# Kernel tuning notes

Measured on AMD Instinct MI355X. Metric: run time of the kernel, lower is better.

## Reference

```python
import jax, jax.numpy as jnp
import numpy as np

N_NODES = 10000
N_EDGES = 320000


def _segment_softmax(scores, seg, num_segments):
    # scores: [E, H], segment-wise stable softmax keyed by seg (edge_index[0])
    m = jax.ops.segment_max(scores, seg, num_segments=num_segments)
    e = jnp.exp(scores - m[seg])
    z = jax.ops.segment_sum(e, seg, num_segments=num_segments)
    return e / z[seg]


def _gat_layer(x, W, a, row, col, n_nodes, heads, out_dim):
    # x: [N, F_in], W: [F_in, heads*out_dim], a: [heads, 2*out_dim]
    h = (x @ W).reshape(n_nodes, heads, out_dim)          # [N, H, F]
    a_l, a_r = a[:, :out_dim], a[:, out_dim:]             # [H, F] each
    # attention score per edge/head without materializing [E, H, 2F]
    s = (h[row] * a_l).sum(-1) + (h[col] * a_r).sum(-1)   # [E, H]
    alpha = _segment_softmax(s, row, n_nodes)             # [E, H]
    msg = alpha[..., None] * h[row]                       # [E, H, F]
    return jax.ops.segment_sum(msg, col, num_segments=n_nodes)  # [N, H, F]


def setup_inputs() -> dict:
    key = jax.random.key(0)
    ks = jax.random.split(key, 6)
    F, H, C = 128, 4, 22
    x = jax.random.normal(ks[0], (N_NODES, F), dtype=jnp.float32)
    edge_index = jax.random.randint(ks[1], (2, N_EDGES), 0, N_NODES, dtype=jnp.int64)
    W1 = jax.random.normal(ks[2], (F, F * H), dtype=jnp.float32) * 0.05
    a1 = jax.random.normal(ks[3], (H, 2 * F), dtype=jnp.float32) * 0.05
    W2 = jax.random.normal(ks[4], (F, C), dtype=jnp.float32) * 0.05
    a2 = jax.random.normal(ks[5], (1, 2 * C), dtype=jnp.float32) * 0.05
    return {"x": x, "edge_index": edge_index, "W1": W1, "a1": a1, "W2": W2, "a2": a2}


def reference(x, edge_index, W1, a1, W2, a2):
    row, col = edge_index[0], edge_index[1]
    h1 = _gat_layer(x, W1, a1, row, col, N_NODES, heads=4, out_dim=128)  # [N, 4, 128]
    h1 = jax.nn.elu(h1).mean(axis=1)                                      # combine heads -> [N, 128]
    h2 = _gat_layer(h1, W2, a2, row, col, N_NODES, heads=1, out_dim=22)   # [N, 1, 22]
    return h2[:, 0, :]                                                    # [N, 22]
```

## Files before the change

kernel.cpp:

```cpp
#include <hip/hip_runtime.h>

#define NN 10000
#define NE 320000
#define EPP 5000
#define NPART 64

typedef short short8 __attribute__((ext_vector_type(8)));
typedef float f32x4 __attribute__((ext_vector_type(4)));

__device__ __forceinline__ unsigned short f2bf(float f) {
    unsigned u = __float_as_uint(f);
    return (unsigned short)((u + 0x7FFFu + ((u >> 16) & 1u)) >> 16);
}
__device__ __forceinline__ float bflo(unsigned v) { return __uint_as_float(v << 16); }
__device__ __forceinline__ float bfhi(unsigned v) { return __uint_as_float(v & 0xffff0000u); }
__device__ __forceinline__ float bf1(unsigned short v) { return __uint_as_float(((unsigned)v) << 16); }

__device__ __forceinline__ int eread(const void* p, int is64, int i) {
    if (is64) return (int)((const long long*)p)[i];
    return ((const int*)p)[i];
}

__device__ __forceinline__ int detect64(const void* ei) {
    const unsigned* idx = (const unsigned*)ei;
    int all0 = 1;
    for (int j = 1; j < 257; j += 2)
        if (idx[j] != 0u) { all0 = 0; break; }
    return all0;
}

__global__ __launch_bounds__(256) void k_pre(const float* __restrict__ x,
                                             unsigned short* __restrict__ xb,
                                             const void* __restrict__ ei,
                                             unsigned short* __restrict__ degp_c,
                                             unsigned short* __restrict__ degp_r,
                                             unsigned* __restrict__ packed_c,
                                             unsigned* __restrict__ packed_r,
                                             const float* __restrict__ W1, const float* __restrict__ a1,
                                             unsigned short* __restrict__ W1t,
                                             float* __restrict__ wrf) {
    __shared__ int sh[NN];
    const int b = blockIdx.x, t = threadIdx.x;
    if (b < 2500) {
        const int g = b * 256 + t;
        const float2 v = *(const float2*)&x[(size_t)g * 2];
        ushort2 o; o.x = f2bf(v.x); o.y = f2bf(v.y);
        *(ushort2*)&xb[(size_t)g * 2] = o;
    } else if (b < 2500 + 2 * NPART) {
        const int is64 = detect64(ei);
        const int isC = (b < 2500 + NPART);
        const int p = isC ? (b - 2500) : (b - 2500 - NPART);
        const int ebase = p * EPP;
        for (int q = t; q < NN; q += 256) sh[q] = 0;
        __syncthreads();
        if (isC) {
            for (int q = t; q < EPP; q += 256) {
                const int e = ebase + q;
                const int c = eread(ei, is64, NE + e);
                const unsigned rk = (unsigned)atomicAdd(&sh[c], 1);
                packed_c[e] = ((unsigned)c << 13) | rk;
            }
            __syncthreads();
            for (int q = t; q < NN; q += 256) degp_c[p * NN + q] = (unsigned short)sh[q];
        } else {
            for (int q = t; q < EPP; q += 256) {
                const int e = ebase + q;
                const int r = eread(ei, is64, e);
                const unsigned rk = (unsigned)atomicAdd(&sh[r], 1);
                packed_r[e] = ((unsigned)r << 13) | rk;
            }
            __syncthreads();
            for (int q = t; q < NN; q += 256) degp_r[p * NN + q] = (unsigned short)sh[q];
        }
    } else if (b < 2500 + 2 * NPART + 256) {
        const int g = (b - 2500 - 2 * NPART) * 256 + t;
        const int h = g >> 14, j = (g >> 7) & 127, k = g & 127;
        W1t[g] = f2bf(W1[(size_t)k * 512 + h * 128 + j]);
    } else {
        const int g = (b - 2500 - 2 * NPART - 256) * 256 + t;
        const int h = g >> 7, k = g & 127;
        const float* wrow = W1 + (size_t)k * 512 + h * 128;
        const float* av = a1 + h * 256 + 128;
        float s = 0.f;
        for (int d = 0; d < 128; d++) s += wrow[d] * av[d];
        wrf[h * 128 + k] = s;
    }
}

__global__ __launch_bounds__(256) void k_psum(const unsigned short* __restrict__ degp_c,
                                              const unsigned short* __restrict__ degp_r,
                                              unsigned short* __restrict__ pfx_c,
                                              unsigned short* __restrict__ pfx_r,
                                              int* __restrict__ deg_c, int* __restrict__ deg_r) {
    const int g = blockIdx.x * 256 + threadIdx.x;
    if (g >= 2 * NN) return;
    const int arr = g / NN, node = g % NN;
    const unsigned short* degp = arr ? degp_r : degp_c;
    unsigned short* pfx = arr ? pfx_r : pfx_c;
    int* tot = arr ? deg_r : deg_c;
    int sum = 0;
#pragma unroll
    for (int p = 0; p < NPART; p++) {
        pfx[p * NN + node] = (unsigned short)sum;
        sum += (int)degp[p * NN + node];
    }
    tot[node] = sum;
}

__device__ void scan_one_1k(const int* __restrict__ deg, int* __restrict__ start, int* ssum) {
    const int t = threadIdx.x;
    int loc[10];
    const int base = t * 10;
    int sum = 0;
#pragma unroll
    for (int j = 0; j < 10; j++) {
        int i = base + j;
        int v = (i < NN) ? deg[i] : 0;
        loc[j] = sum;
        sum += v;
    }
    const int lane = t & 63, w = t >> 6;
    int xi = sum;
#pragma unroll
    for (int off = 1; off < 64; off <<= 1) {
        int y = __shfl_up(xi, off);
        if (lane >= off) xi += y;
    }
    __syncthreads();
    if (lane == 63) ssum[w] = xi;
    __syncthreads();
    int woff = 0;
#pragma unroll
    for (int k = 0; k < 16; k++)
        if (k < w) woff += ssum[k];
    const int excl = woff + xi - sum;
#pragma unroll
    for (int j = 0; j < 10; j++) {
        int i = base + j;
        if (i < NN) start[i] = excl + loc[j];
    }
}

__global__ __launch_bounds__(1024) void k_scan2(const int* __restrict__ deg_c, const int* __restrict__ deg_r,
                                                int* __restrict__ start_c, int* __restrict__ start_r) {
    __shared__ int ssum[16];
    scan_one_1k(deg_c, start_c, ssum);
    __syncthreads();
    scan_one_1k(deg_r, start_r, ssum);
}

__global__ __launch_bounds__(256) void k_build(const unsigned* __restrict__ packed_c,
                                               const unsigned* __restrict__ packed_r,
                                               const unsigned short* __restrict__ pfx_c,
                                               const unsigned short* __restrict__ pfx_r,
                                               const int* __restrict__ start_c, const int* __restrict__ start_r,
                                               int* __restrict__ csrA, int* __restrict__ csrB,
                                               const float* __restrict__ x, const float* __restrict__ wrf,
                                               float* __restrict__ ehr1) {
    __shared__ float ls[512];
    const int b = blockIdx.x, t = threadIdx.x;
    if (b < 1250) {
        const int e = b * 256 + t;
        const int part = e / EPP;
        const unsigned pc = packed_c[e], pr = packed_r[e];
        const int c = (int)(pc >> 13), rkc = (int)(pc & 8191u);
        const int r = (int)(pr >> 13), rkr = (int)(pr & 8191u);
        csrA[start_c[c] + (int)pfx_c[part * NN + c] + rkc] = r;
        csrB[start_r[r] + (int)pfx_r[part * NN + r] + rkr] = c;
    } else {
        const int lane = t & 63, w = t >> 6;
        ls[t] = wrf[t];
        ls[t + 256] = wrf[t + 256];
        __syncthreads();
        const int i = (b - 1250) * 4 + w;
        const float x0 = x[(size_t)i * 128 + lane];
        const float x1 = x[(size_t)i * 128 + 64 + lane];
        float v[4];
#pragma unroll
        for (int h = 0; h < 4; h++)
            v[h] = x0 * ls[h * 128 + lane] + x1 * ls[h * 128 + 64 + lane];
#pragma unroll
        for (int off = 1; off < 64; off <<= 1) {
#pragma unroll
            for (int j = 0; j < 4; j++) v[j] += __shfl_xor(v[j], off);
        }
        if (lane == 0)
            *(float4*)&ehr1[i * 4] = make_float4(__expf(v[0]), __expf(v[1]), __expf(v[2]), __expf(v[3]));
    }
}

__global__ __launch_bounds__(256) void k_z1(const int* __restrict__ start_r, const int* __restrict__ deg_r,
                                            const int* __restrict__ csrB,
                                            const float* __restrict__ ehr1, float* __restrict__ rz1) {
    const int t = threadIdx.x, lane = t & 63, w = t >> 6;
    const int half = lane >> 5, l32 = lane & 31;
    const int i = blockIdx.x * 8 + w * 2 + half;
    const int s0 = start_r[i], d = deg_r[i];
    float zx = 0.f, zy = 0.f, zz = 0.f, zw = 0.f;
    for (int p = s0 + l32; p < s0 + d; p += 32) {
        const int c = csrB[p];
        const float4 v = *(const float4*)&ehr1[c * 4];
        zx += v.x; zy += v.y; zz += v.z; zw += v.w;
    }
#pragma unroll
    for (int off = 1; off < 32; off <<= 1) {
        zx += __shfl_xor(zx, off); zy += __shfl_xor(zy, off);
        zz += __shfl_xor(zz, off); zw += __shfl_xor(zw, off);
    }
    if (l32 == 0)
        *(float4*)&rz1[i * 4] = make_float4(1.f / zx, 1.f / zy, 1.f / zz, 1.f / zw);
}

__global__ __launch_bounds__(256) void k_aggF(const unsigned short* __restrict__ xb,
                                              const float* __restrict__ ehr1, const float* __restrict__ rz1,
                                              const int* __restrict__ start_c, const int* __restrict__ deg_c,
                                              const int* __restrict__ csrA,
                                              const unsigned short* __restrict__ W1t,
                                              const float* __restrict__ W2, const float* __restrict__ a2,
                                              float* __restrict__ h2, float* __restrict__ ehr2) {
    __shared__ unsigned short lx[16 * 512];
    __shared__ float h1f[16 * 128];
    const int t = threadIdx.x, lane = t & 63, w = t >> 6;
    const int n0 = blockIdx.x * 16;

    {
        const int li = lane & 15, g = lane >> 4;
        const int row = w * 4 + g;
        const int i = n0 + row;
        const float4 er4 = *(const float4*)&ehr1[i * 4];
        const int s0 = start_c[i], dg = deg_c[i];
        int m = dg;
        m = max(m, __shfl_xor(m, 16));
        m = max(m, __shfl_xor(m, 32));
        float acc[4][8];
#pragma unroll
        for (int h = 0; h < 4; h++)
#pragma unroll
            for (int d = 0; d < 8; d++) acc[h][d] = 0.f;
        const int niter = (m + 3) >> 2;
        for (int it = 0; it < niter; ++it) {
            const int base = it * 4;
            int rr[4]; uint4 vv[4]; float4 zz[4];
#pragma unroll
            for (int q = 0; q < 4; q++) {
                int p = s0 + base + q;
                if (p >= NE) p = NE - 1;
                rr[q] = csrA[p];
            }
#pragma unroll
            for (int q = 0; q < 4; q++)
                vv[q] = *(const uint4*)&xb[(size_t)rr[q] * 128 + li * 8];
#pragma unroll
            for (int q = 0; q < 4; q++) {
                const float4 z = *(const float4*)&rz1[rr[q] * 4];
                const bool val = (base + q) < dg;
                zz[q] = val ? z : make_float4(0.f, 0.f, 0.f, 0.f);
            }
#pragma unroll
            for (int q = 0; q < 4; q++) {
                float f[8];
                f[0] = bflo(vv[q].x); f[1] = bfhi(vv[q].x);
                f[2] = bflo(vv[q].y); f[3] = bfhi(vv[q].y);
                f[4] = bflo(vv[q].z); f[5] = bfhi(vv[q].z);
                f[6] = bflo(vv[q].w); f[7] = bfhi(vv[q].w);
                const float wz0 = zz[q].x, wz1 = zz[q].y, wz2 = zz[q].z, wz3 = zz[q].w;
#pragma unroll
                for (int d = 0; d < 8; d++) {
                    acc[0][d] += wz0 * f[d];
                    acc[1][d] += wz1 * f[d];
                    acc[2][d] += wz2 * f[d];
                    acc[3][d] += wz3 * f[d];
                }
            }
        }
        const float ef[4] = {er4.x, er4.y, er4.z, er4.w};
#pragma unroll
        for (int h = 0; h < 4; h++) {
            unsigned o[4];
#pragma unroll
            for (int d2 = 0; d2 < 4; d2++) {
                const unsigned lo = f2bf(acc[h][d2 * 2] * ef[h]);
                const unsigned hi = f2bf(acc[h][d2 * 2 + 1] * ef[h]);
                o[d2] = lo | (hi << 16);
            }
            const int f = h * 16 + li;
            const int sc = (f ^ (row & 7)) << 3;
            *(uint4*)&lx[row * 512 + sc] = make_uint4(o[0], o[1], o[2], o[3]);
        }
    }
    __syncthreads();

    {
        const int r16 = lane & 15, grp = lane >> 4;
#pragma unroll
        for (int jj = 0; jj < 2; jj++) {
            const int j = w * 2 + jj;
            f32x4 hm = (f32x4)0.f;
#pragma unroll
            for (int h = 0; h < 4; h++) {
                f32x4 acc = (f32x4)0.f;
#pragma unroll
                for (int kk = 0; kk < 128; kk += 32) {
                    const int f = h * 16 + (kk >> 3) + grp;
                    const int sc = (f ^ (r16 & 7)) << 3;
                    short8 a = *(const short8*)&lx[r16 * 512 + sc];
                    short8 bfr = *(const short8*)&W1t[(size_t)h * 16384 + (j * 16 + r16) * 128 + kk + grp * 8];
                    acc = __builtin_amdgcn_mfma_f32_16x16x32_bf16(a, bfr, acc, 0, 0, 0);
                }
#pragma unroll
                for (int r = 0; r < 4; r++) {
                    const float v = acc[r];
                    hm[r] += (v > 0.f) ? v : (__expf(v) - 1.f);
                }
            }
#pragma unroll
            for (int r = 0; r < 4; r++)
                h1f[(grp * 4 + r) * 128 + j * 16 + r16] = 0.25f * hm[r];
        }
    }
    __syncthreads();

    {
        const int seg = lane >> 5, c = lane & 31;
#pragma unroll
        for (int q = 0; q < 4; q++) {
            const int nl = w * 4 + q;
            const int i = n0 + nl;
            float part = 0.f;
            if (c < 22) {
                const float* hrow = &h1f[nl * 128 + seg * 64];
                const float* wp = &W2[seg * 64 * 22 + c];
                for (int k = 0; k < 64; k++)
                    part += hrow[k] * wp[k * 22];
            }
            part += __shfl_xor(part, 32);
            if (lane < 22) h2[(size_t)i * 22 + lane] = part;
            float pr = (lane < 22) ? part * a2[22 + lane] : 0.f;
#pragma unroll
            for (int off = 1; off < 64; off <<= 1)
                pr += __shfl_xor(pr, off);
            if (lane == 0) ehr2[i] = __expf(pr);
        }
    }
}

__global__ __launch_bounds__(256) void k_z2s(const int* __restrict__ start_r, const int* __restrict__ deg_r,
                                             const int* __restrict__ csrB,
                                             const float* __restrict__ ehr2, const float* __restrict__ h2,
                                             unsigned short* __restrict__ h2s) {
    const int t = threadIdx.x, lane = t & 63, w = t >> 6;
    const int half = lane >> 5, l32 = lane & 31;
    const int i = blockIdx.x * 8 + w * 2 + half;
    const int s0 = start_r[i], d = deg_r[i];
    float z = 0.f;
    for (int p = s0 + l32; p < s0 + d; p += 32)
        z += ehr2[csrB[p]];
#pragma unroll
    for (int off = 1; off < 32; off <<= 1)
        z += __shfl_xor(z, off);
    const float rz = 1.f / z;
    if (l32 < 22)
        h2s[(size_t)i * 32 + l32] = f2bf(h2[(size_t)i * 22 + l32] * rz);
}

__global__ __launch_bounds__(256) void k_agg2(const unsigned short* __restrict__ h2s,
                                              const float* __restrict__ ehr2,
                                              const int* __restrict__ start_c, const int* __restrict__ deg_c,
                                              const int* __restrict__ csrA,
                                              float* __restrict__ out) {
    const int t = threadIdx.x, lane = t & 63, w = t >> 6;
    const int half = lane >> 5, c32 = lane & 31;
    const int i = blockIdx.x * 8 + w * 2 + half;
    const int s0 = start_c[i], dg = deg_c[i];
    const float e2 = ehr2[i];
    const int c = (c32 < 22) ? c32 : 0;
    float acc = 0.f;
    int p = s0;
    const int e8 = s0 + (dg & ~7);
    for (; p < e8; p += 8) {
        int rr[8];
#pragma unroll
        for (int q = 0; q < 8; q++) rr[q] = csrA[p + q];
        float vv[8];
#pragma unroll
        for (int q = 0; q < 8; q++) vv[q] = bf1(h2s[(size_t)rr[q] * 32 + c]);
#pragma unroll
        for (int q = 0; q < 8; q++) acc += vv[q];
    }
    for (; p < s0 + dg; ++p) {
        const int r = csrA[p];
        acc += bf1(h2s[(size_t)r * 32 + c]);
    }
    if (c32 < 22) out[(size_t)i * 22 + c32] = acc * e2;
}

extern "C" void kernel_launch(void* const* d_in, const int* in_sizes, int n_in,
                              void* d_out, int out_size, void* d_ws, size_t ws_size,
                              hipStream_t stream) {
    const float* x  = (const float*)d_in[0];
    const void*  ei = d_in[1];
    const float* W1 = (const float*)d_in[2];
    const float* a1 = (const float*)d_in[3];
    const float* W2 = (const float*)d_in[4];
    const float* a2 = (const float*)d_in[5];
    float* out = (float*)d_out;

    float* ws = (float*)d_ws;
    float* h2   = ws;
    float* ehr1 = ws + 220000;
    float* rz1  = ws + 260000;
    float* ehr2 = ws + 300000;
    unsigned short* h2s = (unsigned short*)(ws + 310000);
    int* deg_c   = (int*)(ws + 470000);
    int* deg_r   = (int*)(ws + 480000);
    int* start_c = (int*)(ws + 490000);
    int* start_r = (int*)(ws + 500000);
    int* csrA    = (int*)(ws + 510000);
    int* csrB    = (int*)(ws + 830000);
    float* wrf   = ws + 1150000;
    unsigned short* W1t = (unsigned short*)(ws + 1151000);
    unsigned short* xb  = (unsigned short*)(ws + 1184000);
    unsigned* packed_c = (unsigned*)(ws + 1824000);
    unsigned* packed_r = (unsigned*)(ws + 2144000);
    unsigned short* degp_c = (unsigned short*)(ws + 2464000);
    unsigned short* degp_r = (unsigned short*)(ws + 2784000);
    unsigned short* pfx_c  = (unsigned short*)(ws + 3104000);
    unsigned short* pfx_r  = (unsigned short*)(ws + 3424000);

    k_pre<<<2500 + 2 * NPART + 258, 256, 0, stream>>>(x, xb, ei, degp_c, degp_r,
                                                      packed_c, packed_r, W1, a1, W1t, wrf);
    k_psum<<<79, 256, 0, stream>>>(degp_c, degp_r, pfx_c, pfx_r, deg_c, deg_r);
    k_scan2<<<1, 1024, 0, stream>>>(deg_c, deg_r, start_c, start_r);
    k_build<<<3750, 256, 0, stream>>>(packed_c, packed_r, pfx_c, pfx_r,
                                      start_c, start_r, csrA, csrB, x, wrf, ehr1);
    k_z1<<<1250, 256, 0, stream>>>(start_r, deg_r, csrB, ehr1, rz1);
    k_aggF<<<625, 256, 0, stream>>>(xb, ehr1, rz1, start_c, deg_c, csrA, W1t,
                                    W2, a2, h2, ehr2);
    k_z2s<<<1250, 256, 0, stream>>>(start_r, deg_r, csrB, ehr2, h2, h2s);
    k_agg2<<<1250, 256, 0, stream>>>(h2s, ehr2, start_c, deg_c, csrA, out);
}
```

Before: 99.33 us.

## Split fused aggregate+GEMM kernel into wave-per-node aggregation and separate GEMM

Splits the fused layer-1 aggregation and MFMA GEMM kernel into two kernels. The new aggregation kernel assigns one wave per destination node and spreads its edges across four 16-lane groups, then combines them with shuffles. This removes the load imbalance of the old scheme, where four nodes shared a wave and each group waited on the maximum degree. The cost is an extra kernel launch plus a bf16 round trip of the aggregated features (10000x512) through global memory before the GEMM kernel reloads them into shared memory.

After: 105.5 us. 1.06x slower.

```diff
diff --git a/kernel.cpp b/kernel.cpp
--- a/kernel.cpp
+++ b/kernel.cpp
@@ -211,82 +211,90 @@
         *(float4*)&rz1[i * 4] = make_float4(1.f / zx, 1.f / zy, 1.f / zz, 1.f / zw);
 }
 
-__global__ __launch_bounds__(256) void k_aggF(const unsigned short* __restrict__ xb,
-                                              const float* __restrict__ ehr1, const float* __restrict__ rz1,
-                                              const int* __restrict__ start_c, const int* __restrict__ deg_c,
-                                              const int* __restrict__ csrA,
-                                              const unsigned short* __restrict__ W1t,
-                                              const float* __restrict__ W2, const float* __restrict__ a2,
-                                              float* __restrict__ h2, float* __restrict__ ehr2) {
+__global__ __launch_bounds__(256) void k_agg1s(const unsigned short* __restrict__ xb,
+                                               const float* __restrict__ ehr1, const float* __restrict__ rz1,
+                                               const int* __restrict__ start_c, const int* __restrict__ deg_c,
+                                               const int* __restrict__ csrA,
+                                               unsigned short* __restrict__ xaggb) {
+    const int t = threadIdx.x, lane = t & 63, w = t >> 6;
+    const int li = lane & 15, g = lane >> 4;
+    const int i = blockIdx.x * 4 + w;
+    const float4 er4 = *(const float4*)&ehr1[i * 4];
+    const int s0 = start_c[i], dg = deg_c[i];
+    float acc[4][8];
+#pragma unroll
+    for (int h = 0; h < 4; h++)
+#pragma unroll
+        for (int d = 0; d < 8; d++) acc[h][d] = 0.f;
+    const int niter = (dg + 7) >> 3;
+    for (int it = 0; it < niter; ++it) {
+        const int base = it * 8 + g * 2;
+        int rr[2]; uint4 vv[2]; float4 zz[2];
+#pragma unroll
+        for (int q = 0; q < 2; q++) {
+            int p = s0 + base + q;
+            if (p >= NE) p = NE - 1;
+            rr[q] = csrA[p];
+        }
+#pragma unroll
+        for (int q = 0; q < 2; q++)
+            vv[q] = *(const uint4*)&xb[(size_t)rr[q] * 128 + li * 8];
+#pragma unroll
+        for (int q = 0; q < 2; q++) {
+            const float4 z = *(const float4*)&rz1[rr[q] * 4];
+            const bool val = (base + q) < dg;
+            zz[q] = val ? z : make_float4(0.f, 0.f, 0.f, 0.f);
+        }
+#pragma unroll
+        for (int q = 0; q < 2; q++) {
+            float f[8];
+            f[0] = bflo(vv[q].x); f[1] = bfhi(vv[q].x);
+            f[2] = bflo(vv[q].y); f[3] = bfhi(vv[q].y);
+            f[4] = bflo(vv[q].z); f[5] = bfhi(vv[q].z);
+            f[6] = bflo(vv[q].w); f[7] = bfhi(vv[q].w);
+            const float wz0 = zz[q].x, wz1 = zz[q].y, wz2 = zz[q].z, wz3 = zz[q].w;
+#pragma unroll
+            for (int d = 0; d < 8; d++) {
+                acc[0][d] += wz0 * f[d];
+                acc[1][d] += wz1 * f[d];
+                acc[2][d] += wz2 * f[d];
+                acc[3][d] += wz3 * f[d];
+            }
+        }
+    }
+#pragma unroll
+    for (int h = 0; h < 4; h++)
+#pragma unroll
+        for (int d = 0; d < 8; d++) {
+            acc[h][d] += __shfl_xor(acc[h][d], 16);
+            acc[h][d] += __shfl_xor(acc[h][d], 32);
+        }
+    const float ef[4] = {er4.x, er4.y, er4.z, er4.w};
+    const int h = g;
+    unsigned o[4];
+#pragma unroll
+    for (int d2 = 0; d2 < 4; d2++) {
+        const unsigned lo = f2bf(acc[h][d2 * 2] * ef[h]);
+        const unsigned hi = f2bf(acc[h][d2 * 2 + 1] * ef[h]);
+        o[d2] = lo | (hi << 16);
+    }
+    *(uint4*)&xaggb[(size_t)i * 512 + h * 128 + li * 8] = make_uint4(o[0], o[1], o[2], o[3]);
+}
+
+__global__ __launch_bounds__(256) void k_gemmFC(const unsigned short* __restrict__ xaggb,
+                                                const unsigned short* __restrict__ W1t,
+                                                const float* __restrict__ W2, const float* __restrict__ a2,
+                                                float* __restrict__ h2, float* __restrict__ ehr2) {
     __shared__ unsigned short lx[16 * 512];
     __shared__ float h1f[16 * 128];
     const int t = threadIdx.x, lane = t & 63, w = t >> 6;
     const int n0 = blockIdx.x * 16;
 
-    {
-        const int li = lane & 15, g = lane >> 4;
-        const int row = w * 4 + g;
-        const int i = n0 + row;
-        const float4 er4 = *(const float4*)&ehr1[i * 4];
-        const int s0 = start_c[i], dg = deg_c[i];
-        int m = dg;
-        m = max(m, __shfl_xor(m, 16));
-        m = max(m, __shfl_xor(m, 32));
-        float acc[4][8];
-#pragma unroll
-        for (int h = 0; h < 4; h++)
-#pragma unroll
-            for (int d = 0; d < 8; d++) acc[h][d] = 0.f;
-        const int niter = (m + 3) >> 2;
-        for (int it = 0; it < niter; ++it) {
-            const int base = it * 4;
-            int rr[4]; uint4 vv[4]; float4 zz[4];
-#pragma unroll
-            for (int q = 0; q < 4; q++) {
-                int p = s0 + base + q;
-                if (p >= NE) p = NE - 1;
-                rr[q] = csrA[p];
-            }
-#pragma unroll
-            for (int q = 0; q < 4; q++)
-                vv[q] = *(const uint4*)&xb[(size_t)rr[q] * 128 + li * 8];
-#pragma unroll
-            for (int q = 0; q < 4; q++) {
-                const float4 z = *(const float4*)&rz1[rr[q] * 4];
-                const bool val = (base + q) < dg;
-                zz[q] = val ? z : make_float4(0.f, 0.f, 0.f, 0.f);
-            }
-#pragma unroll
-            for (int q = 0; q < 4; q++) {
-                float f[8];
-                f[0] = bflo(vv[q].x); f[1] = bfhi(vv[q].x);
-                f[2] = bflo(vv[q].y); f[3] = bfhi(vv[q].y);
-                f[4] = bflo(vv[q].z); f[5] = bfhi(vv[q].z);
-                f[6] = bflo(vv[q].w); f[7] = bfhi(vv[q].w);
-                const float wz0 = zz[q].x, wz1 = zz[q].y, wz2 = zz[q].z, wz3 = zz[q].w;
-#pragma unroll
-                for (int d = 0; d < 8; d++) {
-                    acc[0][d] += wz0 * f[d];
-                    acc[1][d] += wz1 * f[d];
-                    acc[2][d] += wz2 * f[d];
-                    acc[3][d] += wz3 * f[d];
-                }
-            }
-        }
-        const float ef[4] = {er4.x, er4.y, er4.z, er4.w};
-#pragma unroll
-        for (int h = 0; h < 4; h++) {
-            unsigned o[4];
-#pragma unroll
-            for (int d2 = 0; d2 < 4; d2++) {
-                const unsigned lo = f2bf(acc[h][d2 * 2] * ef[h]);
-                const unsigned hi = f2bf(acc[h][d2 * 2 + 1] * ef[h]);
-                o[d2] = lo | (hi << 16);
-            }
-            const int f = h * 16 + li;
-            const int sc = (f ^ (row & 7)) << 3;
-            *(uint4*)&lx[row * 512 + sc] = make_uint4(o[0], o[1], o[2], o[3]);
-        }
+    for (int ff = t; ff < 1024; ff += 256) {
+        const int row = ff >> 6, f = ff & 63;
+        const uint4 v = *(const uint4*)&xaggb[(size_t)(n0 + row) * 512 + f * 8];
+        const int sc = ((f ^ (row & 7)) << 3);
+        *(uint4*)&lx[row * 512 + sc] = v;
     }
     __syncthreads();
 
@@ -426,6 +434,7 @@
     unsigned short* degp_r = (unsigned short*)(ws + 2784000);
     unsigned short* pfx_c  = (unsigned short*)(ws + 3104000);
     unsigned short* pfx_r  = (unsigned short*)(ws + 3424000);
+    unsigned short* xaggb  = (unsigned short*)(ws + 3744000);
 
     k_pre<<<2500 + 2 * NPART + 258, 256, 0, stream>>>(x, xb, ei, degp_c, degp_r,
                                                       packed_c, packed_r, W1, a1, W1t, wrf);
@@ -434,8 +443,8 @@
     k_build<<<3750, 256, 0, stream>>>(packed_c, packed_r, pfx_c, pfx_r,
                                       start_c, start_r, csrA, csrB, x, wrf, ehr1);
     k_z1<<<1250, 256, 0, stream>>>(start_r, deg_r, csrB, ehr1, rz1);
-    k_aggF<<<625, 256, 0, stream>>>(xb, ehr1, rz1, start_c, deg_c, csrA, W1t,
-                                    W2, a2, h2, ehr2);
+    k_agg1s<<<2500, 256, 0, stream>>>(xb, ehr1, rz1, start_c, deg_c, csrA, xaggb);
+    k_gemmFC<<<625, 256, 0, stream>>>(xaggb, W1t, W2, a2, h2, ehr2);
     k_z2s<<<1250, 256, 0, stream>>>(start_r, deg_r, csrB, ehr2, h2, h2s);
     k_agg2<<<1250, 256, 0, stream>>>(h2s, ehr2, start_c, deg_c, csrA, out);
 }
```
